# Performance work log

Hardware: AMD Instinct MI355X
Metric: run time of the kernel (lower is better)

## Reference

```python
import jax, jax.numpy as jnp
import numpy as np

B, T, C, H, N = 4, 1024, 1024, 16, 64  # head_size N = 64 (hardcoded), H = C // N
FFN = 4 * C
EPS = 1e-5
HEAD_DIV = 8.0  # head_size_divisor


def setup_inputs():
    key = jax.random.key(0)
    ks = jax.random.split(key, 24)
    rn = lambda k, sh, s=0.02: jax.random.normal(k, sh, jnp.float32) * s
    ru = lambda k, sh: jax.random.uniform(k, sh, jnp.float32)
    return {
        "x": jax.random.normal(ks[0], (B, T, C), jnp.float32),
        "ln1_w": jnp.ones((C,), jnp.float32), "ln1_b": jnp.zeros((C,), jnp.float32),
        "ln2_w": jnp.ones((C,), jnp.float32), "ln2_b": jnp.zeros((C,), jnp.float32),
        "tm_mix_k": ru(ks[1], (C,)), "tm_mix_v": ru(ks[2], (C,)),
        "tm_mix_r": ru(ks[3], (C,)), "tm_mix_g": ru(ks[4], (C,)),
        "tm_decay": jax.random.uniform(ks[5], (H, N), jnp.float32, -6.0, -1.0),
        "tm_u": rn(ks[6], (H, N), 0.5),
        "Wr": rn(ks[7], (C, C)), "Wk": rn(ks[8], (C, C)), "Wv": rn(ks[9], (C, C)),
        "Wg": rn(ks[10], (C, C)), "Wo": rn(ks[11], (C, C)),
        "lnx_w": jnp.ones((C,), jnp.float32), "lnx_b": jnp.zeros((C,), jnp.float32),
        "cm_mix_k": ru(ks[12], (C,)), "cm_mix_r": ru(ks[13], (C,)),
        "cm_Wk": rn(ks[14], (FFN, C)), "cm_Wr": rn(ks[15], (C, C)), "cm_Wv": rn(ks[16], (C, FFN)),
    }


def _layernorm(x, w, b):
    m = x.mean(-1, keepdims=True)
    v = ((x - m) ** 2).mean(-1, keepdims=True)
    return (x - m) * jax.lax.rsqrt(v + EPS) * w + b


def _time_shift(x):
    # ZeroPad2d((0,0,1,-1)): shift sequence right by one, zero at t=0
    return jnp.concatenate([jnp.zeros_like(x[:, :1]), x[:, :-1]], axis=1)


def _wkv5(r, k, v, w, u):
    # r,k,v: [B,T,H,N]; w,u: [H,N]. Recurrent linear attention per head.
    ew = jnp.exp(-jnp.exp(w))  # decay in (0,1), [H,N]
    ewb = ew[None, :, :, None]  # decay along key dim i of state S[b,h,i,j]
    ub = u[None, :, :, None]

    def step(S, inp):
        rt, kt, vt = inp  # each [B,H,N]
        at = jnp.einsum('bhi,bhj->bhij', kt, vt)           # k_t outer v_t
        yt = jnp.einsum('bhi,bhij->bhj', rt, S + ub * at)   # r_t . (S + u*kv)
        S = ewb * S + at
        return S, yt

    xs = (jnp.swapaxes(r, 0, 1), jnp.swapaxes(k, 0, 1), jnp.swapaxes(v, 0, 1))  # [T,B,H,N]
    S0 = jnp.zeros((r.shape[0], r.shape[2], r.shape[3], v.shape[3]), r.dtype)
    _, ys = jax.lax.scan(step, S0, xs)
    return jnp.swapaxes(ys, 0, 1)  # [B,T,H,N]


def _groupnorm(x, w, b):
    # GroupNorm(H groups) over channel dim per token; x: [B,T,C]
    xh = x.reshape(B, T, H, N)
    m = xh.mean(-1, keepdims=True)
    v = ((xh - m) ** 2).mean(-1, keepdims=True)
    xn = (xh - m) * jax.lax.rsqrt(v + EPS)
    return (xn * w.reshape(H, N) + b.reshape(H, N)).reshape(B, T, C)


def _time_mix(x, tm_mix_k, tm_mix_v, tm_mix_r, tm_mix_g, tm_decay, tm_u,
              Wr, Wk, Wv, Wg, Wo, lnx_w, lnx_b):
    xx = _time_shift(x)
    xk = x * tm_mix_k + xx * (1 - tm_mix_k)
    xv = x * tm_mix_v + xx * (1 - tm_mix_v)
    xr = x * tm_mix_r + xx * (1 - tm_mix_r)
    xg = x * tm_mix_g + xx * (1 - tm_mix_g)
    r = (xr @ Wr.T).reshape(B, T, H, N)
    k = (xk @ Wk.T).reshape(B, T, H, N)
    v = (xv @ Wv.T).reshape(B, T, H, N)
    g = jax.nn.silu(xg @ Wg.T)
    y = _wkv5(r, k, v, tm_decay, tm_u).reshape(B, T, C)
    y = _groupnorm(y / HEAD_DIV, lnx_w, lnx_b)
    return (y * g) @ Wo.T


def _channel_mix(x, cm_mix_k, cm_mix_r, cm_Wk, cm_Wr, cm_Wv):
    xx = _time_shift(x)
    xk = x * cm_mix_k + xx * (1 - cm_mix_k)
    xr = x * cm_mix_r + xx * (1 - cm_mix_r)
    k = jnp.square(jax.nn.relu(xk @ cm_Wk.T))  # [B,T,4C]
    kv = k @ cm_Wv.T
    return jax.nn.sigmoid(xr @ cm_Wr.T) * kv


def reference(x, ln1_w, ln1_b, ln2_w, ln2_b,
              tm_mix_k, tm_mix_v, tm_mix_r, tm_mix_g, tm_decay, tm_u,
              Wr, Wk, Wv, Wg, Wo, lnx_w, lnx_b,
              cm_mix_k, cm_mix_r, cm_Wk, cm_Wr, cm_Wv):
    x = x + _time_mix(_layernorm(x, ln1_w, ln1_b), tm_mix_k, tm_mix_v, tm_mix_r,
                      tm_mix_g, tm_decay, tm_u, Wr, Wk, Wv, Wg, Wo, lnx_w, lnx_b)
    x = x + _channel_mix(_layernorm(x, ln2_w, ln2_b), cm_mix_k, cm_mix_r,
                         cm_Wk, cm_Wr, cm_Wv)
    return x
```

## Files before the change

kernel.cpp:

```cpp
#include <hip/hip_runtime.h>
#include <stdint.h>

typedef unsigned short u16;
typedef __attribute__((ext_vector_type(8))) short short8;
typedef __attribute__((ext_vector_type(4))) float f32x4;

#define BB 4
#define TT 1024
#define CC 1024
#define HH 16
#define NN 64
#define MM (BB*TT)
#define FFN_ 4096
#define PCH 16
#define LCH (TT/PCH)
static constexpr float EPS_ = 1e-5f;

__device__ __forceinline__ u16 f2bf(float f) {
    union { float f; uint32_t u; } x; x.f = f;
    uint32_t r = x.u + 0x7fff + ((x.u >> 16) & 1);
    return (u16)(r >> 16);
}
__device__ __forceinline__ float bf2f(u16 b) {
    union { uint32_t u; float f; } x; x.u = ((uint32_t)b) << 16; return x.f;
}

#define VMW8() asm volatile("s_waitcnt vmcnt(8)" ::: "memory")
#define VMW4() asm volatile("s_waitcnt vmcnt(4)" ::: "memory")
#define VMW0() asm volatile("s_waitcnt vmcnt(0)" ::: "memory")
#define BARRIER() do { asm volatile("" ::: "memory"); __builtin_amdgcn_s_barrier(); asm volatile("" ::: "memory"); } while (0)

__global__ __launch_bounds__(256) void lnz_kernel(const float* __restrict__ x,
    const float* __restrict__ w, const float* __restrict__ b, u16* __restrict__ z)
{
    int row = blockIdx.x;
    int tid = threadIdx.x;
    const float* xr = x + (size_t)row * CC;
    float4 v = ((const float4*)xr)[tid];
    float s  = v.x + v.y + v.z + v.w;
    float ss = v.x*v.x + v.y*v.y + v.z*v.z + v.w*v.w;
#pragma unroll
    for (int m = 1; m < 64; m <<= 1) { s += __shfl_xor(s, m); ss += __shfl_xor(ss, m); }
    __shared__ float as_[4], bs_[4];
    int wv = tid >> 6, ln = tid & 63;
    if (ln == 0) { as_[wv] = s; bs_[wv] = ss; }
    __syncthreads();
    s  = as_[0] + as_[1] + as_[2] + as_[3];
    ss = bs_[0] + bs_[1] + bs_[2] + bs_[3];
    float mean = s * (1.f / CC);
    float var  = ss * (1.f / CC) - mean * mean;
    float inv  = rsqrtf(var + EPS_);
    float4 w4 = ((const float4*)w)[tid];
    float4 b4 = ((const float4*)b)[tid];
    ushort4 o;
    o.x = f2bf((v.x - mean) * inv * w4.x + b4.x);
    o.y = f2bf((v.y - mean) * inv * w4.y + b4.y);
    o.z = f2bf((v.z - mean) * inv * w4.z + b4.z);
    o.w = f2bf((v.w - mean) * inv * w4.w + b4.w);
    int t = row & (TT - 1);
    *(ushort4*)(z + (size_t)row * 2048 + tid * 4) = o;
    if (t < TT - 1) *(ushort4*)(z + (size_t)(row + 1) * 2048 + 1024 + tid * 4) = o;
    if (t == 0) {
        ushort4 zz; zz.x = 0; zz.y = 0; zz.z = 0; zz.w = 0;
        *(ushort4*)(z + (size_t)row * 2048 + 1024 + tid * 4) = zz;
    }
}

__global__ __launch_bounds__(256) void mix2b_kernel(const u16* __restrict__ z2,
    const float* __restrict__ mk, const float* __restrict__ mr,
    u16* __restrict__ xk, u16* __restrict__ xr)
{
    int idx = blockIdx.x * 256 + threadIdx.x;
    int row = idx >> 8, c = (idx & 255) << 2;
    const u16* zr = z2 + (size_t)row * 2048;
    ushort4 zc = *(const ushort4*)(zr + c);
    ushort4 zp = *(const ushort4*)(zr + 1024 + c);
    float xc0 = bf2f(zc.x), xc1 = bf2f(zc.y), xc2 = bf2f(zc.z), xc3 = bf2f(zc.w);
    float xp0 = bf2f(zp.x), xp1 = bf2f(zp.y), xp2 = bf2f(zp.z), xp3 = bf2f(zp.w);
    float4 k4 = *(const float4*)(mk + c);
    float4 r4 = *(const float4*)(mr + c);
    ushort4 ok, orr;
    ok.x  = f2bf(xp0 + k4.x * (xc0 - xp0)); ok.y  = f2bf(xp1 + k4.y * (xc1 - xp1));
    ok.z  = f2bf(xp2 + k4.z * (xc2 - xp2)); ok.w  = f2bf(xp3 + k4.w * (xc3 - xp3));
    orr.x = f2bf(xp0 + r4.x * (xc0 - xp0)); orr.y = f2bf(xp1 + r4.y * (xc1 - xp1));
    orr.z = f2bf(xp2 + r4.z * (xc2 - xp2)); orr.w = f2bf(xp3 + r4.w * (xc3 - xp3));
    size_t f = (size_t)row * 1024 + c;
    *(ushort4*)(xk + f) = ok;
    *(ushort4*)(xr + f) = orr;
}

struct PrepArgs {
    const float *Wr, *Wk, *Wv, *Wg, *mr, *mk, *mv, *mg;
    u16* W4p;
    const float* csrc[4];
    u16* cdst[4];
    int cstart4[4];
    int ctotal4;
};
__global__ __launch_bounds__(256) void prep_kernel(PrepArgs a)
{
    int bid = blockIdx.x;
    if (bid < 4096) {
        int idx = bid * 256 + threadIdx.x;
        int n = idx >> 8, c = (idx & 255) << 2;
        int sel = n >> 10, nr = n & 1023;
        const float* W = sel == 0 ? a.Wr : sel == 1 ? a.Wk : sel == 2 ? a.Wv : a.Wg;
        const float* mx = sel == 0 ? a.mr : sel == 1 ? a.mk : sel == 2 ? a.mv : a.mg;
        float4 w4 = *(const float4*)(W + (size_t)nr * 1024 + c);
        float4 m4 = *(const float4*)(mx + c);
        ushort4 p, q4;
        p.x  = f2bf(w4.x * m4.x); p.y  = f2bf(w4.y * m4.y);
        p.z  = f2bf(w4.z * m4.z); p.w  = f2bf(w4.w * m4.w);
        q4.x = f2bf(w4.x * (1.f - m4.x)); q4.y = f2bf(w4.y * (1.f - m4.y));
        q4.z = f2bf(w4.z * (1.f - m4.z)); q4.w = f2bf(w4.w * (1.f - m4.w));
        *(ushort4*)(a.W4p + (size_t)n * 2048 + c) = p;
        *(ushort4*)(a.W4p + (size_t)n * 2048 + 1024 + c) = q4;
    } else {
        int i4 = (bid - 4096) * 256 + threadIdx.x;
        if (i4 >= a.ctotal4) return;
        int s = 0;
#pragma unroll
        for (int j = 1; j < 4; ++j) if (i4 >= a.cstart4[j]) s = j;
        int l4 = i4 - a.cstart4[s];
        float4 v = ((const float4*)a.csrc[s])[l4];
        ushort4 o; o.x = f2bf(v.x); o.y = f2bf(v.y); o.z = f2bf(v.z); o.w = f2bf(v.w);
        ((ushort4*)a.cdst[s])[l4] = o;
    }
}

__device__ __forceinline__ void stage_tile(const u16* gbase, int rbase, int ldk,
                                           int kcol, u16* ldsbase, int tid)
{
#pragma unroll
    for (int rd = 0; rd < 2; ++rd) {
        int row = rd * 128 + (tid >> 2);
        int slog = (tid & 3) ^ ((row >> 1) & 3);
        const u16* src = gbase + (size_t)(rbase + row) * ldk + kcol + (slog << 3);
        u16* dst = ldsbase + row * 32 + ((tid & 3) << 3);
        __builtin_amdgcn_global_load_lds(
            (const __attribute__((address_space(1))) uint32_t*)(const void*)src,
            (__attribute__((address_space(3))) uint32_t*)(void*)dst, 16, 0, 0);
    }
}

template<int EPI>
__global__ __launch_bounds__(512, 2) void gemm8(
    const u16* __restrict__ A, const u16* __restrict__ Bw,
    float* __restrict__ Cf, u16* __restrict__ Cbf,
    int Mdim, int Ndim, int Kdim, int kLen)
{
    __shared__ u16 As[4 * 8192];
    __shared__ u16 Bs[4 * 8192];
    int tid = threadIdx.x;
    int wid = tid >> 6, lane = tid & 63;
    int wm = wid >> 2, wn = wid & 3;
    int f = lane & 15, g = lane >> 4;

    int nwg = gridDim.x * gridDim.y;
    int bid = blockIdx.y * gridDim.x + blockIdx.x;
    int qq = nwg >> 3, r8 = nwg & 7;
    int xcd = bid & 7, lid = bid >> 3;
    int swz = (xcd < r8 ? xcd * (qq + 1) : r8 * (qq + 1) + (xcd - r8) * qq) + lid;
    int bx = swz % gridDim.x, by = swz / gridDim.x;
    int rowBase = by * 256, colBase = bx * 256;
    int kOff = blockIdx.z * kLen;
    int NT = kLen >> 5;
    if (EPI == 7) Cf += (size_t)blockIdx.z * Mdim * Ndim;

    f32x4 acc[8][4] = {};

    stage_tile(A,  rowBase, Kdim, kOff,      As, tid);
    stage_tile(Bw, colBase, Kdim, kOff,      Bs, tid);
    if (NT > 1) {
        stage_tile(A,  rowBase, Kdim, kOff + 32, As + 8192, tid);
        stage_tile(Bw, colBase, Kdim, kOff + 32, Bs + 8192, tid);
    }
    if (NT > 2) {
        stage_tile(A,  rowBase, Kdim, kOff + 64, As + 2 * 8192, tid);
        stage_tile(Bw, colBase, Kdim, kOff + 64, Bs + 2 * 8192, tid);
    }

    for (int t = 0; t < NT; ++t) {
        if (t < NT - 2) { VMW8(); } else if (t == NT - 2) { VMW4(); } else { VMW0(); }
        BARRIER();
        const u16* Asl = As + (t & 3) * 8192;
        const u16* Bsl = Bs + (t & 3) * 8192;
        short8 bfr[4], afr[4];
#pragma unroll
        for (int n = 0; n < 4; ++n) {
            int row = wn * 64 + n * 16 + f;
            bfr[n] = *(const short8*)(Bsl + row * 32 + ((g ^ ((row >> 1) & 3)) << 3));
        }
#pragma unroll
        for (int m = 0; m < 4; ++m) {
            int row = wm * 128 + m * 16 + f;
            afr[m] = *(const short8*)(Asl + row * 32 + ((g ^ ((row >> 1) & 3)) << 3));
        }
        if (t + 3 < NT)
            stage_tile(A, rowBase, Kdim, kOff + (t + 3) * 32, As + ((t + 3) & 3) * 8192, tid);
        __builtin_amdgcn_s_setprio(1);
#pragma unroll
        for (int m = 0; m < 4; ++m)
#pragma unroll
            for (int n = 0; n < 4; ++n)
                acc[m][n] = __builtin_amdgcn_mfma_f32_16x16x32_bf16(afr[m], bfr[n], acc[m][n], 0, 0, 0);
        __builtin_amdgcn_s_setprio(0);
#pragma unroll
        for (int m = 0; m < 4; ++m) {
            int row = wm * 128 + 64 + m * 16 + f;
            afr[m] = *(const short8*)(Asl + row * 32 + ((g ^ ((row >> 1) & 3)) << 3));
        }
        if (t + 3 < NT)
            stage_tile(Bw, colBase, Kdim, kOff + (t + 3) * 32, Bs + ((t + 3) & 3) * 8192, tid);
        __builtin_amdgcn_s_setprio(1);
#pragma unroll
        for (int m = 0; m < 4; ++m)
#pragma unroll
            for (int n = 0; n < 4; ++n)
                acc[4 + m][n] = __builtin_amdgcn_mfma_f32_16x16x32_bf16(afr[m], bfr[n], acc[4 + m][n], 0, 0, 0);
        __builtin_amdgcn_s_setprio(0);
    }

    int r0 = rowBase + wm * 128, c0 = colBase + wn * 64;
    bool dsilu = (EPI == 6) && (colBase >= 3072);
#pragma unroll
    for (int am = 0; am < 8; ++am) {
#pragma unroll
        for (int n = 0; n < 4; ++n) {
#pragma unroll
            for (int rg = 0; rg < 4; ++rg) {
                int gr = r0 + am * 16 + (lane >> 4) * 4 + rg;
                int gc = c0 + n * 16 + (lane & 15);
                size_t idx = (size_t)gr * Ndim + gc;
                float v = acc[am][n][rg];
                if (EPI == 3) { float rr = v > 0.f ? v : 0.f; Cbf[idx] = f2bf(rr * rr); }
                else if (EPI == 6) Cf[idx] = dsilu ? v / (1.f + __expf(-v)) : v;
                else Cf[idx] = v;
            }
        }
    }
}

__device__ __forceinline__ void stage_tile128(const u16* gbase, int rbase, int ldk,
                                              int kcol, u16* ldsbase, int tid)
{
#pragma unroll
    for (int rd = 0; rd < 2; ++rd) {
        int row = rd * 64 + (tid >> 2);
        int slog = (tid & 3) ^ ((row >> 1) & 3);
        const u16* src = gbase + (size_t)(rbase + row) * ldk + kcol + (slog << 3);
        u16* dst = ldsbase + row * 32 + ((tid & 3) << 3);
        __builtin_amdgcn_global_load_lds(
            (const __attribute__((address_space(1))) uint32_t*)(const void*)src,
            (__attribute__((address_space(3))) uint32_t*)(void*)dst, 16, 0, 0);
    }
}

template<int EPI>
__global__ __launch_bounds__(256, 2) void gemmr(
    const u16* __restrict__ A, const u16* __restrict__ Bw,
    float* __restrict__ Cf,
    const float* __restrict__ aux1,
    int Mdim, int Ndim, int Kdim)
{
    __shared__ u16 As[4 * 4096];
    __shared__ u16 Bs[4 * 4096];
    int tid = threadIdx.x;
    int wid = tid >> 6, lane = tid & 63;
    int wm = wid >> 1, wn = wid & 1;
    int f = lane & 15, g = lane >> 4;

    int nwg = gridDim.x * gridDim.y;
    int bid = blockIdx.y * gridDim.x + blockIdx.x;
    int qq = nwg >> 3, r8 = nwg & 7;
    int xcd = bid & 7, lid = bid >> 3;
    int swz = (xcd < r8 ? xcd * (qq + 1) : r8 * (qq + 1) + (xcd - r8) * qq) + lid;
    int bx = swz % gridDim.x, by = swz / gridDim.x;
    int rowBase = by * 128, colBase = bx * 128;
    int NT = Kdim >> 5;

    f32x4 acc[4][4] = {};

    stage_tile128(A,  rowBase, Kdim, 0,  As, tid);
    stage_tile128(Bw, colBase, Kdim, 0,  Bs, tid);
    stage_tile128(A,  rowBase, Kdim, 32, As + 4096, tid);
    stage_tile128(Bw, colBase, Kdim, 32, Bs + 4096, tid);
    stage_tile128(A,  rowBase, Kdim, 64, As + 2 * 4096, tid);
    stage_tile128(Bw, colBase, Kdim, 64, Bs + 2 * 4096, tid);

    for (int t = 0; t < NT; ++t) {
        if (t < NT - 2) { VMW8(); } else if (t == NT - 2) { VMW4(); } else { VMW0(); }
        BARRIER();
        const u16* Asl = As + (t & 3) * 4096;
        const u16* Bsl = Bs + (t & 3) * 4096;
        short8 bfr[4], afr[4];
#pragma unroll
        for (int n = 0; n < 4; ++n) {
            int row = wn * 64 + n * 16 + f;
            bfr[n] = *(const short8*)(Bsl + row * 32 + ((g ^ ((row >> 1) & 3)) << 3));
        }
#pragma unroll
        for (int m = 0; m < 4; ++m) {
            int row = wm * 64 + m * 16 + f;
            afr[m] = *(const short8*)(Asl + row * 32 + ((g ^ ((row >> 1) & 3)) << 3));
        }
        if (t + 3 < NT) {
            stage_tile128(A,  rowBase, Kdim, (t + 3) * 32, As + ((t + 3) & 3) * 4096, tid);
            stage_tile128(Bw, colBase, Kdim, (t + 3) * 32, Bs + ((t + 3) & 3) * 4096, tid);
        }
        __builtin_amdgcn_s_setprio(1);
#pragma unroll
        for (int m = 0; m < 4; ++m)
#pragma unroll
            for (int n = 0; n < 4; ++n)
                acc[m][n] = __builtin_amdgcn_mfma_f32_16x16x32_bf16(afr[m], bfr[n], acc[m][n], 0, 0, 0);
        __builtin_amdgcn_s_setprio(0);
    }

    int r0 = rowBase + wm * 64, c0 = colBase + wn * 64;
#pragma unroll
    for (int m = 0; m < 4; ++m) {
#pragma unroll
        for (int n = 0; n < 4; ++n) {
#pragma unroll
            for (int rg = 0; rg < 4; ++rg) {
                int gr = r0 + m * 16 + (lane >> 4) * 4 + rg;
                int gc = c0 + n * 16 + (lane & 15);
                size_t idx = (size_t)gr * Ndim + gc;
                float v = acc[m][n][rg];
                if (EPI == 2) Cf[idx] = aux1[idx] + v;
                else Cf[idx] = 1.f / (1.f + __expf(-v));
            }
        }
    }
}

__device__ __forceinline__ size_t sidx(int b, int h, int c, int i, int j) {
    return ((((size_t)b * HH + h) * PCH + c) * NN + i) * NN + j;
}

__global__ __launch_bounds__(64) void wkv_p1(
    const float* __restrict__ k, const float* __restrict__ v,
    const float* __restrict__ decay, float* __restrict__ Sloc, int ld)
{
    int blk = blockIdx.x;
    int c  = blk & (PCH - 1);
    int jb = (blk >> 4) & 3;
    int h  = (blk >> 6) & (HH - 1);
    int b  = blk >> 10;
    int lane = threadIdx.x;
    int jj = lane & 15, g = lane >> 4;
    __shared__ float kbufS[64];
    float S[16], ew[16];
#pragma unroll
    for (int ii = 0; ii < 16; ++ii) {
        int i = g * 16 + ii;
        S[ii] = 0.f;
        ew[ii] = expf(-expf(decay[h * NN + i]));
    }
    const size_t base = ((size_t)b * TT + c * LCH) * ld + h * NN;
    const float* kb = k + base;
    const float* vb = v + base + jb * 16;

    for (int t = 0; t < LCH; ++t) {
        size_t off = (size_t)t * ld;
        float kv_ = kb[off + lane];
        float vv  = vb[off + jj];
        kbufS[lane] = kv_;
        __syncthreads();
        float4 kq[4];
#pragma unroll
        for (int q = 0; q < 4; ++q) kq[q] = ((const float4*)kbufS)[g * 4 + q];
        const float* kf = (const float*)kq;
#pragma unroll
        for (int ii = 0; ii < 16; ++ii)
            S[ii] = fmaf(ew[ii], S[ii], kf[ii] * vv);
        __syncthreads();
    }
#pragma unroll
    for (int ii = 0; ii < 16; ++ii)
        Sloc[sidx(b, h, c, g * 16 + ii, jb * 16 + jj)] = S[ii];
}

__global__ __launch_bounds__(64) void wkv_p2(
    const float* __restrict__ decay,
    const float* __restrict__ Sloc, float* __restrict__ Sst)
{
    int blk = blockIdx.x;
    int jb = blk & 3;
    int h  = (blk >> 2) & (HH - 1);
    int b  = blk >> 6;
    int lane = threadIdx.x;
    int jj = lane & 15, g = lane >> 4;
    float Srun[16], ewL[16];
#pragma unroll
    for (int ii = 0; ii < 16; ++ii) {
        int i = g * 16 + ii;
        Srun[ii] = 0.f;
        ewL[ii] = expf(-expf(decay[h * NN + i]) * (float)LCH);
    }
    int j = jb * 16 + jj;
    for (int c = 0; c < PCH; ++c) {
#pragma unroll
        for (int ii = 0; ii < 16; ++ii) {
            size_t id = sidx(b, h, c, g * 16 + ii, j);
            Sst[id] = Srun[ii];
            Srun[ii] = fmaf(ewL[ii], Srun[ii], Sloc[id]);
        }
    }
}

__global__ __launch_bounds__(64) void wkv_p3(
    const float* __restrict__ r, const float* __restrict__ k, const float* __restrict__ v,
    const float* __restrict__ decay, const float* __restrict__ u,
    const float* __restrict__ Sst, float* __restrict__ y, int ld)
{
    int blk = blockIdx.x;
    int c  = blk & (PCH - 1);
    int jb = (blk >> 4) & 3;
    int h  = (blk >> 6) & (HH - 1);
    int b  = blk >> 10;
    int lane = threadIdx.x;
    int jj = lane & 15, g = lane >> 4;
    __shared__ float rkbuf[128];
    float S[16], uu[16], ew[16];
#pragma unroll
    for (int ii = 0; ii < 16; ++ii) {
        int i = g * 16 + ii;
        S[ii] = Sst[sidx(b, h, c, i, jb * 16 + jj)];
        ew[ii] = expf(-expf(decay[h * NN + i]));
        uu[ii] = u[h * NN + i];
    }
    const size_t base = ((size_t)b * TT + c * LCH) * ld + h * NN;
    const float* rb = r + base;
    const float* kb = k + base;
    const float* vb = v + base + jb * 16;
    float* yb = y + (((size_t)b * TT + c * LCH)) * CC + h * NN + jb * 16;

    for (int t = 0; t < LCH; ++t) {
        size_t off = (size_t)t * ld;
        float rv  = rb[off + lane];
        float kv_ = kb[off + lane];
        float vv  = vb[off + jj];
        rkbuf[2 * lane]     = rv;
        rkbuf[2 * lane + 1] = kv_;
        __syncthreads();
        float acc = 0.f;
        const float2* rk2 = (const float2*)rkbuf;
#pragma unroll
        for (int ii = 0; ii < 16; ++ii) {
            float2 p = rk2[g * 16 + ii];
            float kvv = p.y * vv;
            float t1 = fmaf(uu[ii], kvv, S[ii]);
            acc = fmaf(p.x, t1, acc);
            S[ii] = fmaf(ew[ii], S[ii], kvv);
        }
        acc += __shfl_xor(acc, 16);
        acc += __shfl_xor(acc, 32);
        if (g == 0) yb[(size_t)t * CC + jj] = acc;
        __syncthreads();
    }
}

__global__ __launch_bounds__(256) void gn_kernel(const float* __restrict__ y,
    const float* __restrict__ gsil, const float* __restrict__ w, const float* __restrict__ b,
    u16* __restrict__ og)
{
    int row = blockIdx.x;
    int tid = threadIdx.x;
    int head = tid >> 4, q = tid & 15;
    int cb = head * NN + q * 4;
    size_t base = (size_t)row * CC + cb;
    float4 v = *(const float4*)(y + base);
    v.x *= 0.125f; v.y *= 0.125f; v.z *= 0.125f; v.w *= 0.125f;
    float s  = v.x + v.y + v.z + v.w;
    float ss = v.x*v.x + v.y*v.y + v.z*v.z + v.w*v.w;
#pragma unroll
    for (int m = 1; m < 16; m <<= 1) { s += __shfl_xor(s, m); ss += __shfl_xor(ss, m); }
    float mean = s * (1.f / NN);
    float var  = ss * (1.f / NN) - mean * mean;
    float inv  = rsqrtf(var + EPS_);
    float4 w4 = *(const float4*)(w + cb);
    float4 b4 = *(const float4*)(b + cb);
    float4 g4 = *(const float4*)(gsil + (size_t)row * 4096 + cb);
    ushort4 o;
    o.x = f2bf(((v.x - mean) * inv * w4.x + b4.x) * g4.x);
    o.y = f2bf(((v.y - mean) * inv * w4.y + b4.y) * g4.y);
    o.z = f2bf(((v.z - mean) * inv * w4.z + b4.z) * g4.z);
    o.w = f2bf(((v.w - mean) * inv * w4.w + b4.w) * g4.w);
    *(ushort4*)(og + base) = o;
}

__global__ __launch_bounds__(256) void reduce_cmv(const float* __restrict__ p,
    const float* __restrict__ x1, const float* __restrict__ sr, float* __restrict__ out)
{
    size_t i = ((size_t)blockIdx.x * 256 + threadIdx.x) * 4;
    const size_t stride = (size_t)MM * 1024;
    float4 a0 = *(const float4*)(p + i);
    float4 a1 = *(const float4*)(p + stride + i);
    float4 a2 = *(const float4*)(p + 2 * stride + i);
    float4 a3 = *(const float4*)(p + 3 * stride + i);
    float4 xv = *(const float4*)(x1 + i);
    float4 sv = *(const float4*)(sr + i);
    float4 o;
    o.x = xv.x + sv.x * (a0.x + a1.x + a2.x + a3.x);
    o.y = xv.y + sv.y * (a0.y + a1.y + a2.y + a3.y);
    o.z = xv.z + sv.z * (a0.z + a1.z + a2.z + a3.z);
    o.w = xv.w + sv.w * (a0.w + a1.w + a2.w + a3.w);
    *(float4*)(out + i) = o;
}

extern "C" void kernel_launch(void* const* d_in, const int* in_sizes, int n_in,
                              void* d_out, int out_size, void* d_ws, size_t ws_size,
                              hipStream_t stream)
{
    const float* x       = (const float*)d_in[0];
    const float* ln1_w   = (const float*)d_in[1];
    const float* ln1_b   = (const float*)d_in[2];
    const float* ln2_w   = (const float*)d_in[3];
    const float* ln2_b   = (const float*)d_in[4];
    const float* tm_mix_k= (const float*)d_in[5];
    const float* tm_mix_v= (const float*)d_in[6];
    const float* tm_mix_r= (const float*)d_in[7];
    const float* tm_mix_g= (const float*)d_in[8];
    const float* tm_decay= (const float*)d_in[9];
    const float* tm_u    = (const float*)d_in[10];
    const float* Wr      = (const float*)d_in[11];
    const float* Wk      = (const float*)d_in[12];
    const float* Wv      = (const float*)d_in[13];
    const float* Wg      = (const float*)d_in[14];
    const float* Wo      = (const float*)d_in[15];
    const float* lnx_w   = (const float*)d_in[16];
    const float* lnx_b   = (const float*)d_in[17];
    const float* cm_mix_k= (const float*)d_in[18];
    const float* cm_mix_r= (const float*)d_in[19];
    const float* cm_Wk   = (const float*)d_in[20];
    const float* cm_Wr   = (const float*)d_in[21];
    const float* cm_Wv   = (const float*)d_in[22];

    char* ws = (char*)d_ws;
    auto MB = [](size_t m) { return m * 1024ull * 1024ull; };
    u16*   z      = (u16*)(ws + 0);
    float* rkvg   = (float*)(ws + MB(16));
    float* partials = (float*)(ws + MB(16));
    float* ybuf   = (float*)(ws + MB(80));
    float* sr     = (float*)(ws + MB(80));
    u16*   og     = (u16*)(ws + MB(96));
    u16*   xk     = (u16*)(ws + MB(96));
    u16*   xr     = (u16*)(ws + MB(104));
    float* Sloc   = (float*)(ws + MB(112));
    float* x1     = (float*)(ws + MB(112));
    u16*   W4p    = (u16*)(ws + MB(128));
    float* Sst    = (float*)(ws + MB(128));
    u16*   kbuf2  = (u16*)(ws + MB(128));
    u16*   Wo_b   = (u16*)(ws + MB(160));
    u16*   cmWk_b = (u16*)(ws + MB(162));
    u16*   cmWr_b = (u16*)(ws + MB(170));
    u16*   cmWv_b = (u16*)(ws + MB(172));

    PrepArgs pa;
    pa.Wr = Wr; pa.Wk = Wk; pa.Wv = Wv; pa.Wg = Wg;
    pa.mr = tm_mix_r; pa.mk = tm_mix_k; pa.mv = tm_mix_v; pa.mg = tm_mix_g;
    pa.W4p = W4p;
    pa.csrc[0] = Wo;    pa.cdst[0] = Wo_b;
    pa.csrc[1] = cm_Wk; pa.cdst[1] = cmWk_b;
    pa.csrc[2] = cm_Wr; pa.cdst[2] = cmWr_b;
    pa.csrc[3] = cm_Wv; pa.cdst[3] = cmWv_b;
    int q = (CC * CC) / 4;
    pa.cstart4[0] = 0; pa.cstart4[1] = q; pa.cstart4[2] = 5 * q; pa.cstart4[3] = 6 * q;
    pa.ctotal4 = 10 * q;
    prep_kernel<<<4096 + (10 * q + 255) / 256, 256, 0, stream>>>(pa);

    lnz_kernel<<<MM, 256, 0, stream>>>(x, ln1_w, ln1_b, z);

    gemm8<6><<<dim3(16, 16, 1), 512, 0, stream>>>(z, W4p, rkvg, nullptr, MM, 4096, 2048, 2048);

    wkv_p1<<<BB * HH * 4 * PCH, 64, 0, stream>>>(rkvg + 1024, rkvg + 2048, tm_decay, Sloc, 4096);
    wkv_p2<<<BB * HH * 4, 64, 0, stream>>>(tm_decay, Sloc, Sst);
    wkv_p3<<<BB * HH * 4 * PCH, 64, 0, stream>>>(rkvg, rkvg + 1024, rkvg + 2048,
                                                 tm_decay, tm_u, Sst, ybuf, 4096);

    gn_kernel<<<MM, 256, 0, stream>>>(ybuf, rkvg + 3072, lnx_w, lnx_b, og);

    dim3 gr1(CC / 128, MM / 128);
    gemmr<2><<<gr1, 256, 0, stream>>>(og, Wo_b, x1, x, MM, CC, CC);

    lnz_kernel<<<MM, 256, 0, stream>>>(x1, ln2_w, ln2_b, z);
    mix2b_kernel<<<4096, 256, 0, stream>>>(z, cm_mix_k, cm_mix_r, xk, xr);

    gemm8<3><<<dim3(16, 16, 1), 512, 0, stream>>>(xk, cmWk_b, nullptr, kbuf2, MM, 4096, 1024, 1024);
    gemmr<4><<<gr1, 256, 0, stream>>>(xr, cmWr_b, sr, nullptr, MM, CC, CC);

    gemm8<7><<<dim3(4, 16, 4), 512, 0, stream>>>(kbuf2, cmWv_b, partials, nullptr, MM, 1024, 4096, 1024);

    reduce_cmv<<<4096, 256, 0, stream>>>(partials, x1, sr, (float*)d_out);
}
```

Before: 465.9 us.

## Fuse groupnorm into WKV scan and layernorm into channel-mix shift

The WKV phase-3 kernel now runs one 256-thread block per (batch, head, chunk) covering all four j-slices. It applies groupnorm, scaling and the silu gate inline, writing bf16 output directly, so the fp32 y buffer and the separate gn_kernel launch go away. The second layernorm and the time-shift mix are merged into one kernel that recomputes the previous row's layernorm instead of writing and rereading an intermediate z buffer. The costs are an extra sync and serial normalization work inside the sequential scan loop, fewer total blocks for the scan (1024 instead of 4096), and double-reading x1 rows in the merged layernorm kernel.

```diff
diff --git a/kernel.cpp b/kernel.cpp
--- a/kernel.cpp
+++ b/kernel.cpp
@@ -66,24 +66,56 @@
     }
 }
 
-__global__ __launch_bounds__(256) void mix2b_kernel(const u16* __restrict__ z2,
+__global__ __launch_bounds__(256) void ln2m_kernel(const float* __restrict__ x1,
+    const float* __restrict__ w, const float* __restrict__ b,
     const float* __restrict__ mk, const float* __restrict__ mr,
     u16* __restrict__ xk, u16* __restrict__ xr)
 {
-    int idx = blockIdx.x * 256 + threadIdx.x;
-    int row = idx >> 8, c = (idx & 255) << 2;
-    const u16* zr = z2 + (size_t)row * 2048;
-    ushort4 zc = *(const ushort4*)(zr + c);
-    ushort4 zp = *(const ushort4*)(zr + 1024 + c);
-    float xc0 = bf2f(zc.x), xc1 = bf2f(zc.y), xc2 = bf2f(zc.z), xc3 = bf2f(zc.w);
-    float xp0 = bf2f(zp.x), xp1 = bf2f(zp.y), xp2 = bf2f(zp.z), xp3 = bf2f(zp.w);
+    int row = blockIdx.x;
+    int tid = threadIdx.x;
+    int t = row & (TT - 1);
+    float4 vc = ((const float4*)(x1 + (size_t)row * CC))[tid];
+    float4 vp = make_float4(0.f, 0.f, 0.f, 0.f);
+    if (t) vp = ((const float4*)(x1 + (size_t)(row - 1) * CC))[tid];
+    float sc  = vc.x + vc.y + vc.z + vc.w;
+    float ssc = vc.x*vc.x + vc.y*vc.y + vc.z*vc.z + vc.w*vc.w;
+    float sp  = vp.x + vp.y + vp.z + vp.w;
+    float ssp = vp.x*vp.x + vp.y*vp.y + vp.z*vp.z + vp.w*vp.w;
+#pragma unroll
+    for (int m = 1; m < 64; m <<= 1) {
+        sc += __shfl_xor(sc, m); ssc += __shfl_xor(ssc, m);
+        sp += __shfl_xor(sp, m); ssp += __shfl_xor(ssp, m);
+    }
+    __shared__ float red[4][4];
+    int wv = tid >> 6, ln = tid & 63;
+    if (ln == 0) { red[wv][0] = sc; red[wv][1] = ssc; red[wv][2] = sp; red[wv][3] = ssp; }
+    __syncthreads();
+    sc  = red[0][0] + red[1][0] + red[2][0] + red[3][0];
+    ssc = red[0][1] + red[1][1] + red[2][1] + red[3][1];
+    sp  = red[0][2] + red[1][2] + red[2][2] + red[3][2];
+    ssp = red[0][3] + red[1][3] + red[2][3] + red[3][3];
+    float mc = sc * (1.f / CC);
+    float invc = rsqrtf(ssc * (1.f / CC) - mc * mc + EPS_);
+    float mp = sp * (1.f / CC);
+    float invp = rsqrtf(ssp * (1.f / CC) - mp * mp + EPS_);
+    float4 w4 = ((const float4*)w)[tid];
+    float4 b4 = ((const float4*)b)[tid];
+    int c = tid << 2;
     float4 k4 = *(const float4*)(mk + c);
     float4 r4 = *(const float4*)(mr + c);
+    float lc0 = (vc.x - mc) * invc * w4.x + b4.x;
+    float lc1 = (vc.y - mc) * invc * w4.y + b4.y;
+    float lc2 = (vc.z - mc) * invc * w4.z + b4.z;
+    float lc3 = (vc.w - mc) * invc * w4.w + b4.w;
+    float lp0 = t ? (vp.x - mp) * invp * w4.x + b4.x : 0.f;
+    float lp1 = t ? (vp.y - mp) * invp * w4.y + b4.y : 0.f;
+    float lp2 = t ? (vp.z - mp) * invp * w4.z + b4.z : 0.f;
+    float lp3 = t ? (vp.w - mp) * invp * w4.w + b4.w : 0.f;
     ushort4 ok, orr;
-    ok.x  = f2bf(xp0 + k4.x * (xc0 - xp0)); ok.y  = f2bf(xp1 + k4.y * (xc1 - xp1));
-    ok.z  = f2bf(xp2 + k4.z * (xc2 - xp2)); ok.w  = f2bf(xp3 + k4.w * (xc3 - xp3));
-    orr.x = f2bf(xp0 + r4.x * (xc0 - xp0)); orr.y = f2bf(xp1 + r4.y * (xc1 - xp1));
-    orr.z = f2bf(xp2 + r4.z * (xc2 - xp2)); orr.w = f2bf(xp3 + r4.w * (xc3 - xp3));
+    ok.x  = f2bf(lp0 + k4.x * (lc0 - lp0)); ok.y  = f2bf(lp1 + k4.y * (lc1 - lp1));
+    ok.z  = f2bf(lp2 + k4.z * (lc2 - lp2)); ok.w  = f2bf(lp3 + k4.w * (lc3 - lp3));
+    orr.x = f2bf(lp0 + r4.x * (lc0 - lp0)); orr.y = f2bf(lp1 + r4.y * (lc1 - lp1));
+    orr.z = f2bf(lp2 + r4.z * (lc2 - lp2)); orr.w = f2bf(lp3 + r4.w * (lc3 - lp3));
     size_t f = (size_t)row * 1024 + c;
     *(ushort4*)(xk + f) = ok;
     *(ushort4*)(xr + f) = orr;
@@ -410,24 +442,28 @@
     }
 }
 
-__global__ __launch_bounds__(64) void wkv_p3(
+__global__ __launch_bounds__(256) void wkv_p3g(
     const float* __restrict__ r, const float* __restrict__ k, const float* __restrict__ v,
     const float* __restrict__ decay, const float* __restrict__ u,
-    const float* __restrict__ Sst, float* __restrict__ y, int ld)
+    const float* __restrict__ Sst, const float* __restrict__ gsil,
+    const float* __restrict__ gw, const float* __restrict__ gb,
+    u16* __restrict__ og, int ld)
 {
     int blk = blockIdx.x;
-    int c  = blk & (PCH - 1);
-    int jb = (blk >> 4) & 3;
-    int h  = (blk >> 6) & (HH - 1);
-    int b  = blk >> 10;
-    int lane = threadIdx.x;
+    int c = blk & (PCH - 1);
+    int h = (blk >> 4) & (HH - 1);
+    int b = blk >> 8;
+    int tid = threadIdx.x;
+    int jb = tid >> 6, lane = tid & 63;
     int jj = lane & 15, g = lane >> 4;
     __shared__ float rkbuf[128];
+    __shared__ float ysh[64];
     float S[16], uu[16], ew[16];
+    int j = jb * 16 + jj;
 #pragma unroll
     for (int ii = 0; ii < 16; ++ii) {
         int i = g * 16 + ii;
-        S[ii] = Sst[sidx(b, h, c, i, jb * 16 + jj)];
+        S[ii] = Sst[sidx(b, h, c, i, j)];
         ew[ii] = expf(-expf(decay[h * NN + i]));
         uu[ii] = u[h * NN + i];
     }
@@ -435,15 +471,20 @@
     const float* rb = r + base;
     const float* kb = k + base;
     const float* vb = v + base + jb * 16;
-    float* yb = y + (((size_t)b * TT + c * LCH)) * CC + h * NN + jb * 16;
+    float wv_ = gw[h * NN + lane];
+    float bv_ = gb[h * NN + lane];
+    const float* gsb = gsil + ((size_t)b * TT + c * LCH) * 4096 + h * NN;
+    u16* ogb = og + ((size_t)b * TT + c * LCH) * CC + h * NN;
 
     for (int t = 0; t < LCH; ++t) {
         size_t off = (size_t)t * ld;
-        float rv  = rb[off + lane];
-        float kv_ = kb[off + lane];
-        float vv  = vb[off + jj];
-        rkbuf[2 * lane]     = rv;
-        rkbuf[2 * lane + 1] = kv_;
+        float vv = vb[off + jj];
+        if (jb == 0) {
+            float rv  = rb[off + lane];
+            float kv_ = kb[off + lane];
+            rkbuf[2 * lane]     = rv;
+            rkbuf[2 * lane + 1] = kv_;
+        }
         __syncthreads();
         float acc = 0.f;
         const float2* rk2 = (const float2*)rkbuf;
@@ -457,38 +498,21 @@
         }
         acc += __shfl_xor(acc, 16);
         acc += __shfl_xor(acc, 32);
-        if (g == 0) yb[(size_t)t * CC + jj] = acc;
+        if (g == 0) ysh[jb * 16 + jj] = acc;
         __syncthreads();
-    }
-}
-
-__global__ __launch_bounds__(256) void gn_kernel(const float* __restrict__ y,
-    const float* __restrict__ gsil, const float* __restrict__ w, const float* __restrict__ b,
-    u16* __restrict__ og)
-{
-    int row = blockIdx.x;
-    int tid = threadIdx.x;
-    int head = tid >> 4, q = tid & 15;
-    int cb = head * NN + q * 4;
-    size_t base = (size_t)row * CC + cb;
-    float4 v = *(const float4*)(y + base);
-    v.x *= 0.125f; v.y *= 0.125f; v.z *= 0.125f; v.w *= 0.125f;
-    float s  = v.x + v.y + v.z + v.w;
-    float ss = v.x*v.x + v.y*v.y + v.z*v.z + v.w*v.w;
-#pragma unroll
-    for (int m = 1; m < 16; m <<= 1) { s += __shfl_xor(s, m); ss += __shfl_xor(ss, m); }
-    float mean = s * (1.f / NN);
-    float var  = ss * (1.f / NN) - mean * mean;
-    float inv  = rsqrtf(var + EPS_);
-    float4 w4 = *(const float4*)(w + cb);
-    float4 b4 = *(const float4*)(b + cb);
-    float4 g4 = *(const float4*)(gsil + (size_t)row * 4096 + cb);
-    ushort4 o;
-    o.x = f2bf(((v.x - mean) * inv * w4.x + b4.x) * g4.x);
-    o.y = f2bf(((v.y - mean) * inv * w4.y + b4.y) * g4.y);
-    o.z = f2bf(((v.z - mean) * inv * w4.z + b4.z) * g4.z);
-    o.w = f2bf(((v.w - mean) * inv * w4.w + b4.w) * g4.w);
-    *(ushort4*)(og + base) = o;
+        if (jb == 0) {
+            float yv = ysh[lane] * 0.125f;
+            float s = yv, ss = yv * yv;
+#pragma unroll
+            for (int m = 1; m < 64; m <<= 1) { s += __shfl_xor(s, m); ss += __shfl_xor(ss, m); }
+            float mean = s * (1.f / NN);
+            float var  = ss * (1.f / NN) - mean * mean;
+            float inv  = rsqrtf(var + EPS_);
+            float gv = gsb[(size_t)t * 4096 + lane];
+            ogb[(size_t)t * CC + lane] = f2bf(((yv - mean) * inv * wv_ + bv_) * gv);
+        }
+        __syncthreads();
+    }
 }
 
 __global__ __launch_bounds__(256) void reduce_cmv(const float* __restrict__ p,
@@ -543,7 +567,6 @@
     u16*   z      = (u16*)(ws + 0);
     float* rkvg   = (float*)(ws + MB(16));
     float* partials = (float*)(ws + MB(16));
-    float* ybuf   = (float*)(ws + MB(80));
     float* sr     = (float*)(ws + MB(80));
     u16*   og     = (u16*)(ws + MB(96));
     u16*   xk     = (u16*)(ws + MB(96));
@@ -577,16 +600,14 @@
 
     wkv_p1<<<BB * HH * 4 * PCH, 64, 0, stream>>>(rkvg + 1024, rkvg + 2048, tm_decay, Sloc, 4096);
     wkv_p2<<<BB * HH * 4, 64, 0, stream>>>(tm_decay, Sloc, Sst);
-    wkv_p3<<<BB * HH * 4 * PCH, 64, 0, stream>>>(rkvg, rkvg + 1024, rkvg + 2048,
-                                                 tm_decay, tm_u, Sst, ybuf, 4096);
-
-    gn_kernel<<<MM, 256, 0, stream>>>(ybuf, rkvg + 3072, lnx_w, lnx_b, og);
+    wkv_p3g<<<BB * HH * PCH, 256, 0, stream>>>(rkvg, rkvg + 1024, rkvg + 2048,
+                                               tm_decay, tm_u, Sst, rkvg + 3072,
+                                               lnx_w, lnx_b, og, 4096);
 
     dim3 gr1(CC / 128, MM / 128);
     gemmr<2><<<gr1, 256, 0, stream>>>(og, Wo_b, x1, x, MM, CC, CC);
 
-    lnz_kernel<<<MM, 256, 0, stream>>>(x1, ln2_w, ln2_b, z);
-    mix2b_kernel<<<4096, 256, 0, stream>>>(z, cm_mix_k, cm_mix_r, xk, xr);
+    ln2m_kernel<<<MM, 256, 0, stream>>>(x1, ln2_w, ln2_b, cm_mix_k, cm_mix_r, xk, xr);
 
     gemm8<3><<<dim3(16, 16, 1), 512, 0, stream>>>(xk, cmWk_b, nullptr, kbuf2, MM, 4096, 1024, 1024);
     gemmr<4><<<gr1, 256, 0, stream>>>(xr, cmWr_b, sr, nullptr, MM, CC, CC);
```

New measurement: 477.8 us. +2.6%, slower.
